# Kernel optimization log

Hardware: AMD Instinct MI355X
Metric: run time of the kernel (lower is better)

The kernel has to match this reference:

```python
import jax, jax.numpy as jnp
import numpy as np

N_HEAD = 16
TOPK = 2


def _forward(x, noise, Wk, Wv, Wq, Wo, Wg, Wn):
    B, T, C = x.shape
    E = Wg.shape[1]
    H = N_HEAD
    D = C // H
    x2 = x.reshape(-1, C)  # [N, C], N = B*T
    # noisy gating: logits + randn * softplus(noise_proj)
    gate_logits = x2 @ Wg + noise * jax.nn.softplus(x2 @ Wn)  # [N, E]
    w, sel = jax.lax.top_k(gate_logits, TOPK)                 # [N, K]
    w = jax.nn.softmax(w.astype(jnp.float32), axis=1).astype(x.dtype)
    # shared keys/values across experts
    k = (x @ Wk).reshape(B, T, H, D)
    v = (x @ Wv).reshape(B, T, H, D)
    # per-expert queries for all tokens, gathered per selected expert below
    q_all = jnp.einsum('btc,eco->bteo', x, Wq)  # [B, T, E, C]
    causal = jnp.tril(jnp.ones((T, T), dtype=bool))  # key j visible to query t iff j <= t
    scale = 1.0 / np.sqrt(D).astype(np.float32)
    sel_bt = sel.reshape(B, T, TOPK)
    w_bt = w.reshape(B, T, TOPK)
    out = jnp.zeros_like(x)
    for s in range(TOPK):  # small fixed loop over top-k slots
        e = sel_bt[:, :, s]  # [B, T] expert id per token
        q = jnp.take_along_axis(q_all, e[:, :, None, None], axis=2)[:, :, 0, :]  # [B, T, C]
        qh = q.reshape(B, T, H, D)
        scores = jnp.einsum('bthd,bjhd->bhtj', qh, k) * scale  # [B, H, T, T]
        scores = jnp.where(causal[None, None], scores, -jnp.inf)
        p = jax.nn.softmax(scores, axis=-1)
        attn = jnp.einsum('bhtj,bjhd->bthd', p, v).reshape(B, T, C)
        o_all = jnp.einsum('btc,eco->bteo', attn, Wo)  # [B, T, E, C]
        o = jnp.take_along_axis(o_all, e[:, :, None, None], axis=2)[:, :, 0, :]
        out = out + w_bt[:, :, s:s + 1] * o
    return out


def setup_inputs() -> dict:
    key = jax.random.key(0)
    ks = jax.random.split(key, 8)
    B, T, C, E = 4, 1024, 1024, 8
    s = 0.02
    x = jax.random.normal(ks[0], (B, T, C), jnp.float32)
    noise = jax.random.normal(ks[1], (B * T, E), jnp.float32)
    Wk = jax.random.normal(ks[2], (C, C), jnp.float32) * s
    Wv = jax.random.normal(ks[3], (C, C), jnp.float32) * s
    Wq = jax.random.normal(ks[4], (E, C, C), jnp.float32) * s
    Wo = jax.random.normal(ks[5], (E, C, C), jnp.float32) * s
    Wg = jax.random.normal(ks[6], (C, E), jnp.float32) * s
    Wn = jax.random.normal(ks[7], (C, E), jnp.float32) * s
    return {'x': x, 'noise': noise, 'Wk': Wk, 'Wv': Wv, 'Wq': Wq, 'Wo': Wo, 'Wg': Wg, 'Wn': Wn}


def reference(x, noise, Wk, Wv, Wq, Wo, Wg, Wn):
    return _forward(x, noise, Wk, Wv, Wq, Wo, Wg, Wn)
```

## Files before the change

kernel.cpp:

```cpp
#include <hip/hip_runtime.h>
#include <hip/hip_bf16.h>

#define TSEQ   1024
#define NC     1024
#define MBT    4096
#define NEXP   8
#define NHEAD  16
#define DHEAD  64
#define PERM_CAP 10240
#define MAXTILES 96

typedef __attribute__((ext_vector_type(8))) short bf16x8;
typedef __attribute__((ext_vector_type(4))) float f32x4;

typedef __attribute__((address_space(3))) unsigned char* lds_ptr_t;
typedef const __attribute__((address_space(1))) unsigned char* glb_ptr_t;

static __device__ __forceinline__ void gload16(const void* g, void* l){
    __builtin_amdgcn_global_load_lds((glb_ptr_t)g, (lds_ptr_t)l, 16, 0, 0);
}

static __device__ __forceinline__ unsigned short f2bf(float x){
    unsigned int u = __float_as_uint(x);
    u += 0x7fff + ((u >> 16) & 1);
    return (unsigned short)(u >> 16);
}
static __device__ __forceinline__ unsigned int pk2bf(float a, float b){
    unsigned int ua = __float_as_uint(a), ub = __float_as_uint(b);
    ua += 0x7fff + ((ua >> 16) & 1);
    ub += 0x7fff + ((ub >> 16) & 1);
    return (ua >> 16) | (ub & 0xffff0000u);
}

__global__ __launch_bounds__(64)
void gate_kernel(const float* __restrict__ x, const float* __restrict__ noise,
                 const float* __restrict__ Wg, const float* __restrict__ Wn,
                 int* __restrict__ epair, float* __restrict__ wpair,
                 unsigned short* __restrict__ xb){
    int t = blockIdx.x;
    int lane = threadIdx.x;
    float ag[8] = {0,0,0,0,0,0,0,0};
    float an[8] = {0,0,0,0,0,0,0,0};
    const float* xr = x + (size_t)t * NC;
    unsigned short* xbr = xb + (size_t)t * NC;
    for (int c = lane; c < NC; c += 64){
        float xv = xr[c];
        xbr[c] = f2bf(xv);
        #pragma unroll
        for (int j = 0; j < 8; j++){
            ag[j] = fmaf(xv, Wg[c*8 + j], ag[j]);
            an[j] = fmaf(xv, Wn[c*8 + j], an[j]);
        }
    }
    #pragma unroll
    for (int j = 0; j < 8; j++){
        #pragma unroll
        for (int o = 32; o >= 1; o >>= 1){
            ag[j] += __shfl_xor(ag[j], o, 64);
            an[j] += __shfl_xor(an[j], o, 64);
        }
    }
    if (lane == 0){
        float lg[8];
        #pragma unroll
        for (int j = 0; j < 8; j++){
            float z = an[j];
            float sp = (z > 20.f) ? z : log1pf(expf(z));
            lg[j] = ag[j] + noise[(size_t)t*8 + j] * sp;
        }
        int i0 = 0; float v0 = lg[0];
        #pragma unroll
        for (int j = 1; j < 8; j++) if (lg[j] > v0){ v0 = lg[j]; i0 = j; }
        int i1 = -1; float v1 = -3.4e38f;
        #pragma unroll
        for (int j = 0; j < 8; j++) if (j != i0 && lg[j] > v1){ v1 = lg[j]; i1 = j; }
        float e1 = expf(v1 - v0);
        float w0 = 1.f / (1.f + e1);
        epair[2*t]   = i0;
        epair[2*t+1] = i1;
        wpair[2*t]   = w0;
        wpair[2*t+1] = e1 * w0;
    }
}

__global__ void prep_w(const float* __restrict__ Wk, const float* __restrict__ Wv,
                       const float* __restrict__ Wq, const float* __restrict__ Wo,
                       unsigned short* __restrict__ Wkvt, unsigned short* __restrict__ Wqt,
                       unsigned short* __restrict__ Wot){
    __shared__ float t[32][33];
    int z = blockIdx.z;
    const float* src; unsigned short* dst;
    if (z == 0){ src = Wk; dst = Wkvt; }
    else if (z == 1){ src = Wv; dst = Wkvt + (size_t)NC*NC; }
    else if (z < 10){ src = Wq + (size_t)(z-2)*NC*NC; dst = Wqt + (size_t)(z-2)*NC*NC; }
    else { src = Wo + (size_t)(z-10)*NC*NC; dst = Wot + (size_t)(z-10)*NC*NC; }
    int k0 = blockIdx.x * 32, n0 = blockIdx.y * 32;
    int tx = threadIdx.x, ty = threadIdx.y;
    #pragma unroll
    for (int i = 0; i < 4; i++)
        t[ty + i*8][tx] = src[(size_t)(k0 + ty + i*8)*NC + n0 + tx];
    __syncthreads();
    #pragma unroll
    for (int i = 0; i < 4; i++)
        dst[(size_t)(n0 + ty + i*8)*NC + k0 + tx] = f2bf(t[tx][ty + i*8]);
}

__global__ void transpose_v(const unsigned short* __restrict__ kvb, unsigned short* __restrict__ vbT){
    __shared__ unsigned short sh[32][33];
    int b = blockIdx.z;
    int c0 = blockIdx.x * 32, t0 = blockIdx.y * 32;
    int tx = threadIdx.x, ty = threadIdx.y;
    #pragma unroll
    for (int i = 0; i < 4; i++)
        sh[ty + i*8][tx] = kvb[((size_t)(b*TSEQ + t0 + ty + i*8))*2048 + 1024 + c0 + tx];
    __syncthreads();
    #pragma unroll
    for (int i = 0; i < 4; i++){
        int c = c0 + ty + i*8;
        vbT[((size_t)(b*NC + c))*TSEQ + t0 + tx] = sh[tx][ty + i*8];
    }
}

__global__ void group_build(const int* __restrict__ epair, int* __restrict__ cursor,
                            int* __restrict__ tile_g, int* __restrict__ tile_pos,
                            int* __restrict__ ntiles, int* __restrict__ perm){
    __shared__ int cnt[16];
    int tid = threadIdx.x;
    if (tid < 16) cnt[tid] = 0;
    __syncthreads();
    for (int p = tid; p < 2*MBT; p += 256){
        int g = ((p & 1) << 3) | epair[p];
        atomicAdd(&cnt[g], 1);
    }
    for (int i = tid; i < PERM_CAP; i += 256) perm[i] = -1;
    __syncthreads();
    if (tid == 0){
        int off = 0, tt = 0;
        for (int g = 0; g < 16; g++){
            int c = cnt[g];
            cursor[g] = off;
            int nt = (c + 127) >> 7;
            for (int i = 0; i < nt; i++){ tile_g[tt] = g; tile_pos[tt] = off + i*128; tt++; }
            off += nt << 7;
        }
        ntiles[0] = tt;
    }
}

__global__ __launch_bounds__(256)
void fill_perm(const int* __restrict__ epair, int* __restrict__ cursor,
               int* __restrict__ perm){
    int p = blockIdx.x * 256 + threadIdx.x;
    int lane = threadIdx.x & 63;
    int g = ((p & 1) << 3) | epair[p];
    unsigned long long ltmask = (lane == 63) ? 0x7fffffffffffffffull
                                             : (((unsigned long long)1 << lane) - 1);
    #pragma unroll 1
    for (int grp = 0; grp < 16; grp++){
        unsigned long long m = __ballot(g == grp);
        if (m == 0ull) continue;
        if (g == grp){
            int leader = __ffsll(m) - 1;
            int base = 0;
            if (lane == leader) base = atomicAdd(&cursor[grp], __popcll(m));
            base = __shfl(base, leader, 64);
            perm[base + __popcll(m & ltmask)] = p;
        }
    }
}

__global__ __launch_bounds__(256)
void gemm_fused(const unsigned short* __restrict__ xb,
                const unsigned short* __restrict__ Wkvt,
                const unsigned short* __restrict__ Wqt,
                unsigned short* __restrict__ kvbuf,
                unsigned short* __restrict__ qselb,
                const int* __restrict__ perm,
                const int* __restrict__ tile_g,
                const int* __restrict__ tile_pos,
                const int* __restrict__ ntiles){
    int flat = blockIdx.x;
    bool isQ = (flat >= 512);
    int ntile, slot, tpos = 0;
    const unsigned short* bt;
    if (!isQ){
        ntile = flat & 15; slot = flat >> 4;
        bt = Wkvt;
    } else {
        int f2 = flat - 512;
        ntile = f2 & 7; slot = f2 >> 3;
        if (slot >= ntiles[0]) return;
        int g = tile_g[slot];
        bt = Wqt + (size_t)(g & 7) * NC * NC;
        tpos = tile_pos[slot];
    }

    __shared__ __align__(16) unsigned short As[128*64];
    __shared__ __align__(16) unsigned short Bs[128*64];
    int tid = threadIdx.x;
    int lane = tid & 63, wv = tid >> 6;
    int wr = wv >> 1, wc = wv & 1;
    int quad = lane >> 4, l15 = lane & 15;

    int laneR = lane >> 3;
    int swz = ((lane & 7) ^ (laneR & 7)) * 8;

    const unsigned short* ag[4];
    const unsigned short* bg[4];
    #pragma unroll
    for (int it = 0; it < 4; it++){
        int row = wv*32 + it*8 + laneR;
        if (!isQ){
            ag[it] = xb + (size_t)(slot*128 + row) * NC + swz;
        } else {
            int p = perm[tpos + row];
            if (p < 0) p = 0;
            ag[it] = xb + (size_t)(p >> 1) * NC + swz;
        }
        bg[it] = bt + (size_t)(ntile*128 + row) * NC + swz;
    }

    f32x4 acc[4][4];
    #pragma unroll
    for (int i = 0; i < 4; i++)
        #pragma unroll
        for (int j = 0; j < 4; j++) acc[i][j] = (f32x4){0.f,0.f,0.f,0.f};

    for (int kk = 0; kk < NC; kk += 64){
        #pragma unroll
        for (int it = 0; it < 4; it++){
            gload16(ag[it] + kk, &As[(wv*32 + it*8)*64]);
            gload16(bg[it] + kk, &Bs[(wv*32 + it*8)*64]);
        }
        __syncthreads();
        #pragma unroll
        for (int kh = 0; kh < 2; kh++){
            bf16x8 af[4], bfr[4];
            #pragma unroll
            for (int mi = 0; mi < 4; mi++)
                af[mi]  = *(const bf16x8*)&As[(wr*64 + mi*16 + l15)*64 + (((kh*4 + quad) ^ (l15 & 7))*8)];
            #pragma unroll
            for (int ni = 0; ni < 4; ni++)
                bfr[ni] = *(const bf16x8*)&Bs[(wc*64 + ni*16 + l15)*64 + (((kh*4 + quad) ^ (l15 & 7))*8)];
            #pragma unroll
            for (int mi = 0; mi < 4; mi++)
                #pragma unroll
                for (int ni = 0; ni < 4; ni++)
                    acc[mi][ni] = __builtin_amdgcn_mfma_f32_16x16x32_bf16(af[mi], bfr[ni], acc[mi][ni], 0, 0, 0);
        }
        __syncthreads();
    }

    int colbase = ntile*128 + wc*64 + l15;
    #pragma unroll
    for (int mi = 0; mi < 4; mi++){
        #pragma unroll
        for (int r = 0; r < 4; r++){
            int m = wr*64 + mi*16 + quad*4 + r;
            if (!isQ){
                unsigned short* co = kvbuf + (size_t)(slot*128 + m) * 2048 + colbase;
                #pragma unroll
                for (int ni = 0; ni < 4; ni++) co[ni*16] = f2bf(acc[mi][ni][r]);
            } else {
                int p = perm[tpos + m];
                if (p >= 0){
                    unsigned short* co = qselb + (size_t)p * NC + colbase;
                    #pragma unroll
                    for (int ni = 0; ni < 4; ni++) co[ni*16] = f2bf(0.125f * acc[mi][ni][r]);
                }
            }
        }
    }
}

__global__ __launch_bounds__(256)
void gemm_o(const unsigned short* __restrict__ A,
            const unsigned short* __restrict__ Bt,
            float* __restrict__ Cout,
            const int* __restrict__ perm,
            const int* __restrict__ tile_g,
            const int* __restrict__ tile_pos,
            const int* __restrict__ ntiles,
            const float* __restrict__ wpair){
    int ntile = blockIdx.x;
    int slot  = blockIdx.y;
    if (slot >= ntiles[0]) return;
    int g = tile_g[slot];
    const unsigned short* bt = Bt + (size_t)(g & 7) * NC * NC;
    int tpos = tile_pos[slot];

    __shared__ __align__(16) unsigned short As[128*64];
    __shared__ __align__(16) unsigned short Bs[128*64];
    int tid = threadIdx.x;
    int lane = tid & 63, wv = tid >> 6;
    int wr = wv >> 1, wc = wv & 1;
    int quad = lane >> 4, l15 = lane & 15;

    int laneR = lane >> 3;
    int swz = ((lane & 7) ^ (laneR & 7)) * 8;

    const unsigned short* ag[4];
    const unsigned short* bg[4];
    #pragma unroll
    for (int it = 0; it < 4; it++){
        int row = wv*32 + it*8 + laneR;
        int p = perm[tpos + row];
        if (p < 0) p = 0;
        ag[it] = A + (size_t)(p & 1) * MBT * NC + (size_t)(p >> 1) * NC + swz;
        bg[it] = bt + (size_t)(ntile*128 + row) * NC + swz;
    }

    f32x4 acc[4][4];
    #pragma unroll
    for (int i = 0; i < 4; i++)
        #pragma unroll
        for (int j = 0; j < 4; j++) acc[i][j] = (f32x4){0.f,0.f,0.f,0.f};

    for (int kk = 0; kk < NC; kk += 64){
        #pragma unroll
        for (int it = 0; it < 4; it++){
            gload16(ag[it] + kk, &As[(wv*32 + it*8)*64]);
            gload16(bg[it] + kk, &Bs[(wv*32 + it*8)*64]);
        }
        __syncthreads();
        #pragma unroll
        for (int kh = 0; kh < 2; kh++){
            bf16x8 af[4], bfr[4];
            #pragma unroll
            for (int mi = 0; mi < 4; mi++)
                af[mi]  = *(const bf16x8*)&As[(wr*64 + mi*16 + l15)*64 + (((kh*4 + quad) ^ (l15 & 7))*8)];
            #pragma unroll
            for (int ni = 0; ni < 4; ni++)
                bfr[ni] = *(const bf16x8*)&Bs[(wc*64 + ni*16 + l15)*64 + (((kh*4 + quad) ^ (l15 & 7))*8)];
            #pragma unroll
            for (int mi = 0; mi < 4; mi++)
                #pragma unroll
                for (int ni = 0; ni < 4; ni++)
                    acc[mi][ni] = __builtin_amdgcn_mfma_f32_16x16x32_bf16(af[mi], bfr[ni], acc[mi][ni], 0, 0, 0);
        }
        __syncthreads();
    }

    int colbase = ntile*128 + wc*64 + l15;
    #pragma unroll
    for (int mi = 0; mi < 4; mi++){
        #pragma unroll
        for (int r = 0; r < 4; r++){
            int m = wr*64 + mi*16 + quad*4 + r;
            int p = perm[tpos + m];
            if (p >= 0){
                float w = wpair[p];
                float* co = Cout + (size_t)(p & 1) * MBT * NC + (size_t)(p >> 1) * NC + colbase;
                #pragma unroll
                for (int ni = 0; ni < 4; ni++) co[ni*16] = w * acc[mi][ni][r];
            }
        }
    }
}

__global__ void combine(const float* __restrict__ os, float* __restrict__ out){
    size_t i = ((size_t)blockIdx.x * 256 + threadIdx.x) * 4;
    float4 a = *(const float4*)(os + i);
    float4 b = *(const float4*)(os + (size_t)MBT*NC + i);
    float4 r; r.x = a.x+b.x; r.y = a.y+b.y; r.z = a.z+b.z; r.w = a.w+b.w;
    *(float4*)(out + i) = r;
}

__global__ __launch_bounds__(256)
void attn_k(const unsigned short* __restrict__ qsel, const unsigned short* __restrict__ kvb,
            const unsigned short* __restrict__ vbT, unsigned short* __restrict__ attnb){
    int b = blockIdx.y >> 4, h = blockIdx.y & 15;
    int s = blockIdx.z;
    int tid = threadIdx.x, lane = tid & 63, wv = tid >> 6;
    int quad = lane >> 4, l15 = lane & 15;
    int laneR = lane >> 3;
    int swz = ((lane & 7) ^ (laneR & 7)) * 8;

    __shared__ __align__(16) unsigned short ksh[64*64];
    __shared__ __align__(16) unsigned short vsh[64*64];
    __shared__ __align__(16) unsigned short pwork[4][32][72];

    #pragma unroll
    for (int half = 0; half < 2; half++){
        int qb = half ? (7 - blockIdx.x) : blockIdx.x;
        int qbase = qb*128 + wv*32;
        int ig[2] = { qbase + l15, qbase + 16 + l15 };

        bf16x8 qf[2][2];
        #pragma unroll
        for (int isub = 0; isub < 2; isub++){
            const unsigned short* qrow = qsel + (((size_t)(b*TSEQ + qbase + isub*16 + l15))*2 + s)*NC + h*DHEAD;
            qf[isub][0] = *(const bf16x8*)(qrow + quad*8);
            qf[isub][1] = *(const bf16x8*)(qrow + 32 + quad*8);
        }

        float lrun[2] = {0.f, 0.f};
        f32x4 oacc[4][2];
        #pragma unroll
        for (int d = 0; d < 4; d++)
            #pragma unroll
            for (int i = 0; i < 2; i++) oacc[d][i] = (f32x4){0.f,0.f,0.f,0.f};

        int njt = qb*2 + 2;
        for (int jt = 0; jt < njt; jt++){
            #pragma unroll
            for (int it = 0; it < 2; it++){
                int r = wv*16 + it*8 + laneR;
                gload16(kvb + ((size_t)(b*TSEQ + jt*64 + r))*2048 + h*DHEAD + swz,
                        &ksh[(wv*16 + it*8)*64]);
                gload16(vbT + ((size_t)(b*NC + h*DHEAD + r))*TSEQ + jt*64 + swz,
                        &vsh[(wv*16 + it*8)*64]);
            }
            __syncthreads();

            if (jt*64 <= qbase + 31){
                f32x4 sac[4][2];
                #pragma unroll
                for (int jsub = 0; jsub < 4; jsub++){
                    bf16x8 kf0 = *(const bf16x8*)&ksh[(jsub*16 + l15)*64 + ((quad     ^ (l15 & 7))*8)];
                    bf16x8 kf1 = *(const bf16x8*)&ksh[(jsub*16 + l15)*64 + (((4+quad) ^ (l15 & 7))*8)];
                    #pragma unroll
                    for (int isub = 0; isub < 2; isub++){
                        f32x4 z = (f32x4){0.f,0.f,0.f,0.f};
                        z = __builtin_amdgcn_mfma_f32_16x16x32_bf16(kf0, qf[isub][0], z, 0, 0, 0);
                        z = __builtin_amdgcn_mfma_f32_16x16x32_bf16(kf1, qf[isub][1], z, 0, 0, 0);
                        sac[jsub][isub] = z;
                    }
                }
                if (jt*64 + 63 > qbase){
                    #pragma unroll
                    for (int jsub = 0; jsub < 4; jsub++)
                        #pragma unroll
                        for (int r = 0; r < 4; r++){
                            int j = jt*64 + jsub*16 + quad*4 + r;
                            #pragma unroll
                            for (int isub = 0; isub < 2; isub++)
                                if (j > ig[isub]) sac[jsub][isub][r] = -1e30f;
                        }
                }
                #pragma unroll
                for (int isub = 0; isub < 2; isub++){
                    float rs = 0.f;
                    #pragma unroll
                    for (int jsub = 0; jsub < 4; jsub++){
                        float p0 = __expf(sac[jsub][isub][0]);
                        float p1 = __expf(sac[jsub][isub][1]);
                        float p2 = __expf(sac[jsub][isub][2]);
                        float p3 = __expf(sac[jsub][isub][3]);
                        rs += (p0 + p1) + (p2 + p3);
                        uint2 pk;
                        pk.x = pk2bf(p0, p1);
                        pk.y = pk2bf(p2, p3);
                        *(uint2*)&pwork[wv][isub*16 + l15][jsub*16 + quad*4] = pk;
                    }
                    rs += __shfl_xor(rs, 16, 64);
                    rs += __shfl_xor(rs, 32, 64);
                    lrun[isub] += rs;
                }
                bf16x8 pf[2][2];
                #pragma unroll
                for (int kh = 0; kh < 2; kh++)
                    #pragma unroll
                    for (int isub = 0; isub < 2; isub++)
                        pf[kh][isub] = *(const bf16x8*)&pwork[wv][isub*16 + l15][kh*32 + quad*8];
                #pragma unroll
                for (int dsub = 0; dsub < 4; dsub++){
                    bf16x8 vf0 = *(const bf16x8*)&vsh[(dsub*16 + l15)*64 + ((quad     ^ (l15 & 7))*8)];
                    bf16x8 vf1 = *(const bf16x8*)&vsh[(dsub*16 + l15)*64 + (((4+quad) ^ (l15 & 7))*8)];
                    #pragma unroll
                    for (int isub = 0; isub < 2; isub++){
                        oacc[dsub][isub] = __builtin_amdgcn_mfma_f32_16x16x32_bf16(vf0, pf[0][isub], oacc[dsub][isub], 0, 0, 0);
                        oacc[dsub][isub] = __builtin_amdgcn_mfma_f32_16x16x32_bf16(vf1, pf[1][isub], oacc[dsub][isub], 0, 0, 0);
                    }
                }
            }
            __syncthreads();
        }

        float inv[2] = { 1.f / lrun[0], 1.f / lrun[1] };
        #pragma unroll
        for (int dsub = 0; dsub < 4; dsub++)
            #pragma unroll
            for (int isub = 0; isub < 2; isub++){
                uint2 ov;
                ov.x = pk2bf(oacc[dsub][isub][0] * inv[isub], oacc[dsub][isub][1] * inv[isub]);
                ov.y = pk2bf(oacc[dsub][isub][2] * inv[isub], oacc[dsub][isub][3] * inv[isub]);
                *(uint2*)&pwork[wv][isub*16 + l15][dsub*16 + quad*4] = ov;
            }
        #pragma unroll
        for (int rr = 0; rr < 4; rr++){
            int idx = rr*64 + lane;
            int il = idx >> 3, cc = (idx & 7) * 8;
            int t = qb*128 + wv*32 + il;
            *(uint4*)(attnb + (size_t)s*MBT*NC + ((size_t)(b*TSEQ + t))*NC + h*DHEAD + cc) =
                *(const uint4*)&pwork[wv][il][cc];
        }
    }
}

extern "C" void kernel_launch(void* const* d_in, const int* in_sizes, int n_in,
                              void* d_out, int out_size, void* d_ws, size_t ws_size,
                              hipStream_t stream){
    (void)in_sizes; (void)n_in; (void)out_size; (void)ws_size;
    const float* x     = (const float*)d_in[0];
    const float* noise = (const float*)d_in[1];
    const float* Wk    = (const float*)d_in[2];
    const float* Wv    = (const float*)d_in[3];
    const float* Wq    = (const float*)d_in[4];
    const float* Wo    = (const float*)d_in[5];
    const float* Wg    = (const float*)d_in[6];
    const float* Wn    = (const float*)d_in[7];
    float* out = (float*)d_out;

    char* ws = (char*)d_ws;
    size_t off = 0;
    auto alloc = [&](size_t bytes) -> void* {
        void* p = ws + off;
        off += (bytes + 255) & ~(size_t)255;
        return p;
    };
    unsigned short* xb    = (unsigned short*)alloc((size_t)MBT*NC*2);
    unsigned short* vbufT = (unsigned short*)alloc((size_t)MBT*NC*2);
    unsigned short* kvbuf = (unsigned short*)alloc((size_t)MBT*2048*2);
    unsigned short* qselb = (unsigned short*)alloc((size_t)MBT*2*NC*2);
    unsigned short* attnb = (unsigned short*)alloc((size_t)2*MBT*NC*2);
    unsigned short* Wkvt  = (unsigned short*)alloc((size_t)2*NC*NC*2);
    unsigned short* Wqt   = (unsigned short*)alloc((size_t)NEXP*NC*NC*2);
    unsigned short* Wot   = (unsigned short*)alloc((size_t)NEXP*NC*NC*2);
    int*   epair   = (int*)alloc(2*MBT*4);
    float* wpair   = (float*)alloc(2*MBT*4);
    int*   perm    = (int*)alloc(PERM_CAP*4);
    int*   cursor  = (int*)alloc(16*4);
    int*   tile_g  = (int*)alloc(MAXTILES*4);
    int*   tile_pos= (int*)alloc(MAXTILES*4);
    int*   ntiles  = (int*)alloc(4);

    float* osbuf = (float*)kvbuf;

    prep_w<<<dim3(32,32,18), dim3(32,8), 0, stream>>>(Wk, Wv, Wq, Wo, Wkvt, Wqt, Wot);
    gate_kernel<<<4096, 64, 0, stream>>>(x, noise, Wg, Wn, epair, wpair, xb);
    group_build<<<1, 256, 0, stream>>>(epair, cursor, tile_g, tile_pos, ntiles, perm);
    fill_perm<<<32, 256, 0, stream>>>(epair, cursor, perm);

    gemm_fused<<<1280, 256, 0, stream>>>(xb, Wkvt, Wqt, kvbuf, qselb,
                                         perm, tile_g, tile_pos, ntiles);
    transpose_v<<<dim3(32,32,4), dim3(32,8), 0, stream>>>(kvbuf, vbufT);

    attn_k<<<dim3(4,64,2), 256, 0, stream>>>(qselb, kvbuf, vbufT, attnb);

    gemm_o<<<dim3(8,MAXTILES), 256, 0, stream>>>(attnb, Wot, osbuf, perm, tile_g, tile_pos, ntiles, wpair);
    combine<<<4096, 256, 0, stream>>>(osbuf, out);
}
```

Measured before the change: 364.2 us.

## Fuse V transpose into GEMM epilogue, stage stores through LDS, bf16 output partials

The QKV GEMM epilogue now stages each tile in shared memory and writes 16-byte coalesced rows. For V tiles it writes the transposed layout directly, which removes the separate transpose_v kernel. The output-projection GEMM stores bf16 partials, reusing the qsel buffer, instead of fp32 ones, and the gate weights move into the combine kernel. This halves partial-sum traffic. The gate kernel packs four tokens per block. Rounding the O-projection partials to bf16 adds some precision loss.

```diff
diff --git a/kernel.cpp b/kernel.cpp
--- a/kernel.cpp
+++ b/kernel.cpp
@@ -31,14 +31,17 @@
     ub += 0x7fff + ((ub >> 16) & 1);
     return (ua >> 16) | (ub & 0xffff0000u);
 }
-
-__global__ __launch_bounds__(64)
+static __device__ __forceinline__ float bf2f(unsigned short u){
+    return __uint_as_float(((unsigned int)u) << 16);
+}
+
+__global__ __launch_bounds__(256)
 void gate_kernel(const float* __restrict__ x, const float* __restrict__ noise,
                  const float* __restrict__ Wg, const float* __restrict__ Wn,
                  int* __restrict__ epair, float* __restrict__ wpair,
                  unsigned short* __restrict__ xb){
-    int t = blockIdx.x;
-    int lane = threadIdx.x;
+    int t = blockIdx.x*4 + (threadIdx.x >> 6);
+    int lane = threadIdx.x & 63;
     float ag[8] = {0,0,0,0,0,0,0,0};
     float an[8] = {0,0,0,0,0,0,0,0};
     const float* xr = x + (size_t)t * NC;
@@ -103,22 +106,6 @@
     #pragma unroll
     for (int i = 0; i < 4; i++)
         dst[(size_t)(n0 + ty + i*8)*NC + k0 + tx] = f2bf(t[tx][ty + i*8]);
-}
-
-__global__ void transpose_v(const unsigned short* __restrict__ kvb, unsigned short* __restrict__ vbT){
-    __shared__ unsigned short sh[32][33];
-    int b = blockIdx.z;
-    int c0 = blockIdx.x * 32, t0 = blockIdx.y * 32;
-    int tx = threadIdx.x, ty = threadIdx.y;
-    #pragma unroll
-    for (int i = 0; i < 4; i++)
-        sh[ty + i*8][tx] = kvb[((size_t)(b*TSEQ + t0 + ty + i*8))*2048 + 1024 + c0 + tx];
-    __syncthreads();
-    #pragma unroll
-    for (int i = 0; i < 4; i++){
-        int c = c0 + ty + i*8;
-        vbT[((size_t)(b*NC + c))*TSEQ + t0 + tx] = sh[tx][ty + i*8];
-    }
 }
 
 __global__ void group_build(const int* __restrict__ epair, int* __restrict__ cursor,
@@ -173,7 +160,8 @@
 void gemm_fused(const unsigned short* __restrict__ xb,
                 const unsigned short* __restrict__ Wkvt,
                 const unsigned short* __restrict__ Wqt,
-                unsigned short* __restrict__ kvbuf,
+                unsigned short* __restrict__ kbuf,
+                unsigned short* __restrict__ vbT,
                 unsigned short* __restrict__ qselb,
                 const int* __restrict__ perm,
                 const int* __restrict__ tile_g,
@@ -195,8 +183,10 @@
         tpos = tile_pos[slot];
     }
 
-    __shared__ __align__(16) unsigned short As[128*64];
-    __shared__ __align__(16) unsigned short Bs[128*64];
+    __shared__ __align__(16) unsigned short smem[16896];
+    unsigned short* As = smem;
+    unsigned short* Bs = smem + 8192;
+
     int tid = threadIdx.x;
     int lane = tid & 63, wv = tid >> 6;
     int wr = wv >> 1, wc = wv & 1;
@@ -251,24 +241,52 @@
         __syncthreads();
     }
 
-    int colbase = ntile*128 + wc*64 + l15;
-    #pragma unroll
-    for (int mi = 0; mi < 4; mi++){
-        #pragma unroll
-        for (int r = 0; r < 4; r++){
-            int m = wr*64 + mi*16 + quad*4 + r;
+    bool isV = (!isQ) && (ntile >= 8);
+    float scale = isQ ? 0.125f : 1.0f;
+    if (!isV){
+        #pragma unroll
+        for (int mi = 0; mi < 4; mi++)
+            #pragma unroll
+            for (int ni = 0; ni < 4; ni++)
+                #pragma unroll
+                for (int r = 0; r < 4; r++)
+                    smem[(wr*64 + mi*16 + quad*4 + r)*132 + wc*64 + ni*16 + l15] =
+                        f2bf(scale * acc[mi][ni][r]);
+        __syncthreads();
+        #pragma unroll
+        for (int cc = 0; cc < 8; cc++){
+            int chunk = tid + cc*256;
+            int row = chunk >> 4, c8 = (chunk & 15) * 8;
+            uint4 v = *(const uint4*)&smem[row*132 + c8];
             if (!isQ){
-                unsigned short* co = kvbuf + (size_t)(slot*128 + m) * 2048 + colbase;
-                #pragma unroll
-                for (int ni = 0; ni < 4; ni++) co[ni*16] = f2bf(acc[mi][ni][r]);
+                *(uint4*)(kbuf + (size_t)(slot*128 + row)*NC + ntile*128 + c8) = v;
             } else {
-                int p = perm[tpos + m];
-                if (p >= 0){
-                    unsigned short* co = qselb + (size_t)p * NC + colbase;
-                    #pragma unroll
-                    for (int ni = 0; ni < 4; ni++) co[ni*16] = f2bf(0.125f * acc[mi][ni][r]);
-                }
+                int p = perm[tpos + row];
+                if (p >= 0)
+                    *(uint4*)(qselb + (size_t)p*NC + ntile*128 + c8) = v;
             }
+        }
+    } else {
+        #pragma unroll
+        for (int mi = 0; mi < 4; mi++)
+            #pragma unroll
+            for (int ni = 0; ni < 4; ni++){
+                ushort4 pk;
+                pk.x = f2bf(acc[mi][ni][0]);
+                pk.y = f2bf(acc[mi][ni][1]);
+                pk.z = f2bf(acc[mi][ni][2]);
+                pk.w = f2bf(acc[mi][ni][3]);
+                *(ushort4*)&smem[(wc*64 + ni*16 + l15)*132 + wr*64 + mi*16 + quad*4] = pk;
+            }
+        __syncthreads();
+        int b = slot >> 3, t0 = (slot & 7)*128;
+        int cvBase = (ntile - 8)*128;
+        #pragma unroll
+        for (int cc = 0; cc < 8; cc++){
+            int chunk = tid + cc*256;
+            int row = chunk >> 4, c8 = (chunk & 15) * 8;
+            uint4 v = *(const uint4*)&smem[row*132 + c8];
+            *(uint4*)(vbT + ((size_t)(b*NC + cvBase + row))*TSEQ + t0 + c8) = v;
         }
     }
 }
@@ -276,12 +294,11 @@
 __global__ __launch_bounds__(256)
 void gemm_o(const unsigned short* __restrict__ A,
             const unsigned short* __restrict__ Bt,
-            float* __restrict__ Cout,
+            unsigned short* __restrict__ osb,
             const int* __restrict__ perm,
             const int* __restrict__ tile_g,
             const int* __restrict__ tile_pos,
-            const int* __restrict__ ntiles,
-            const float* __restrict__ wpair){
+            const int* __restrict__ ntiles){
     int ntile = blockIdx.x;
     int slot  = blockIdx.y;
     if (slot >= ntiles[0]) return;
@@ -289,8 +306,10 @@
     const unsigned short* bt = Bt + (size_t)(g & 7) * NC * NC;
     int tpos = tile_pos[slot];
 
-    __shared__ __align__(16) unsigned short As[128*64];
-    __shared__ __align__(16) unsigned short Bs[128*64];
+    __shared__ __align__(16) unsigned short smem[16896];
+    unsigned short* As = smem;
+    unsigned short* Bs = smem + 8192;
+
     int tid = threadIdx.x;
     int lane = tid & 63, wv = tid >> 6;
     int wr = wv >> 1, wc = wv & 1;
@@ -341,33 +360,50 @@
         __syncthreads();
     }
 
-    int colbase = ntile*128 + wc*64 + l15;
-    #pragma unroll
-    for (int mi = 0; mi < 4; mi++){
-        #pragma unroll
-        for (int r = 0; r < 4; r++){
-            int m = wr*64 + mi*16 + quad*4 + r;
-            int p = perm[tpos + m];
-            if (p >= 0){
-                float w = wpair[p];
-                float* co = Cout + (size_t)(p & 1) * MBT * NC + (size_t)(p >> 1) * NC + colbase;
-                #pragma unroll
-                for (int ni = 0; ni < 4; ni++) co[ni*16] = w * acc[mi][ni][r];
-            }
-        }
-    }
-}
-
-__global__ void combine(const float* __restrict__ os, float* __restrict__ out){
-    size_t i = ((size_t)blockIdx.x * 256 + threadIdx.x) * 4;
-    float4 a = *(const float4*)(os + i);
-    float4 b = *(const float4*)(os + (size_t)MBT*NC + i);
-    float4 r; r.x = a.x+b.x; r.y = a.y+b.y; r.z = a.z+b.z; r.w = a.w+b.w;
-    *(float4*)(out + i) = r;
+    #pragma unroll
+    for (int mi = 0; mi < 4; mi++)
+        #pragma unroll
+        for (int ni = 0; ni < 4; ni++)
+            #pragma unroll
+            for (int r = 0; r < 4; r++)
+                smem[(wr*64 + mi*16 + quad*4 + r)*132 + wc*64 + ni*16 + l15] =
+                    f2bf(acc[mi][ni][r]);
+    __syncthreads();
+    #pragma unroll
+    for (int cc = 0; cc < 8; cc++){
+        int chunk = tid + cc*256;
+        int row = chunk >> 4, c8 = (chunk & 15) * 8;
+        int p = perm[tpos + row];
+        if (p >= 0){
+            uint4 v = *(const uint4*)&smem[row*132 + c8];
+            *(uint4*)(osb + ((size_t)(p & 1)*MBT + (p >> 1))*NC + ntile*128 + c8) = v;
+        }
+    }
 }
 
 __global__ __launch_bounds__(256)
-void attn_k(const unsigned short* __restrict__ qsel, const unsigned short* __restrict__ kvb,
+void combine(const unsigned short* __restrict__ os, const float* __restrict__ wpair,
+             float* __restrict__ out){
+    size_t flat = ((size_t)blockIdx.x * 256 + threadIdx.x) * 8;
+    int t = (int)(flat >> 10);
+    float w0 = wpair[2*t], w1 = wpair[2*t+1];
+    bf16x8 a = *(const bf16x8*)(os + flat);
+    bf16x8 b = *(const bf16x8*)(os + (size_t)MBT*NC + flat);
+    float4 r0, r1;
+    r0.x = w0*bf2f((unsigned short)a[0]) + w1*bf2f((unsigned short)b[0]);
+    r0.y = w0*bf2f((unsigned short)a[1]) + w1*bf2f((unsigned short)b[1]);
+    r0.z = w0*bf2f((unsigned short)a[2]) + w1*bf2f((unsigned short)b[2]);
+    r0.w = w0*bf2f((unsigned short)a[3]) + w1*bf2f((unsigned short)b[3]);
+    r1.x = w0*bf2f((unsigned short)a[4]) + w1*bf2f((unsigned short)b[4]);
+    r1.y = w0*bf2f((unsigned short)a[5]) + w1*bf2f((unsigned short)b[5]);
+    r1.z = w0*bf2f((unsigned short)a[6]) + w1*bf2f((unsigned short)b[6]);
+    r1.w = w0*bf2f((unsigned short)a[7]) + w1*bf2f((unsigned short)b[7]);
+    *(float4*)(out + flat)     = r0;
+    *(float4*)(out + flat + 4) = r1;
+}
+
+__global__ __launch_bounds__(256)
+void attn_k(const unsigned short* __restrict__ qsel, const unsigned short* __restrict__ kb,
             const unsigned short* __restrict__ vbT, unsigned short* __restrict__ attnb){
     int b = blockIdx.y >> 4, h = blockIdx.y & 15;
     int s = blockIdx.z;
@@ -406,7 +442,7 @@
             #pragma unroll
             for (int it = 0; it < 2; it++){
                 int r = wv*16 + it*8 + laneR;
-                gload16(kvb + ((size_t)(b*TSEQ + jt*64 + r))*2048 + h*DHEAD + swz,
+                gload16(kb  + ((size_t)(b*TSEQ + jt*64 + r))*NC + h*DHEAD + swz,
                         &ksh[(wv*16 + it*8)*64]);
                 gload16(vbT + ((size_t)(b*NC + h*DHEAD + r))*TSEQ + jt*64 + swz,
                         &vsh[(wv*16 + it*8)*64]);
@@ -521,7 +557,7 @@
     };
     unsigned short* xb    = (unsigned short*)alloc((size_t)MBT*NC*2);
     unsigned short* vbufT = (unsigned short*)alloc((size_t)MBT*NC*2);
-    unsigned short* kvbuf = (unsigned short*)alloc((size_t)MBT*2048*2);
+    unsigned short* kbuf  = (unsigned short*)alloc((size_t)MBT*NC*2);
     unsigned short* qselb = (unsigned short*)alloc((size_t)MBT*2*NC*2);
     unsigned short* attnb = (unsigned short*)alloc((size_t)2*MBT*NC*2);
     unsigned short* Wkvt  = (unsigned short*)alloc((size_t)2*NC*NC*2);
@@ -535,19 +571,18 @@
     int*   tile_pos= (int*)alloc(MAXTILES*4);
     int*   ntiles  = (int*)alloc(4);
 
-    float* osbuf = (float*)kvbuf;
+    unsigned short* osb = qselb;
 
     prep_w<<<dim3(32,32,18), dim3(32,8), 0, stream>>>(Wk, Wv, Wq, Wo, Wkvt, Wqt, Wot);
-    gate_kernel<<<4096, 64, 0, stream>>>(x, noise, Wg, Wn, epair, wpair, xb);
+    gate_kernel<<<1024, 256, 0, stream>>>(x, noise, Wg, Wn, epair, wpair, xb);
     group_build<<<1, 256, 0, stream>>>(epair, cursor, tile_g, tile_pos, ntiles, perm);
     fill_perm<<<32, 256, 0, stream>>>(epair, cursor, perm);
 
-    gemm_fused<<<1280, 256, 0, stream>>>(xb, Wkvt, Wqt, kvbuf, qselb,
+    gemm_fused<<<1280, 256, 0, stream>>>(xb, Wkvt, Wqt, kbuf, vbufT, qselb,
                                          perm, tile_g, tile_pos, ntiles);
-    transpose_v<<<dim3(32,32,4), dim3(32,8), 0, stream>>>(kvbuf, vbufT);
-
-    attn_k<<<dim3(4,64,2), 256, 0, stream>>>(qselb, kvbuf, vbufT, attnb);
-
-    gemm_o<<<dim3(8,MAXTILES), 256, 0, stream>>>(attnb, Wot, osbuf, perm, tile_g, tile_pos, ntiles, wpair);
-    combine<<<4096, 256, 0, stream>>>(osbuf, out);
-}
+
+    attn_k<<<dim3(4,64,2), 256, 0, stream>>>(qselb, kbuf, vbufT, attnb);
+
+    gemm_o<<<dim3(8,MAXTILES), 256, 0, stream>>>(attnb, Wot, osb, perm, tile_g, tile_pos, ntiles);
+    combine<<<2048, 256, 0, stream>>>(osb, wpair, out);
+}
```

New measurement: 347.0 us. 4.7% less time.
